# Kernel optimization log

Measured on AMD Instinct MI355X. Metric: run time of the kernel, lower is better.

Reference implementation:

```python
import jax, jax.numpy as jnp
import numpy as np

N, E = 50000, 500000
D_NODE, D_EDGE, N_REL, N_CLS = 128, 128, 64, 16


def setup_inputs() -> dict:
    key = jax.random.key(0)
    ks = jax.random.split(key, 16)
    cat = 2 * D_NODE + D_EDGE  # 384
    s = 0.05
    return {
        "node_features": jax.random.normal(ks[0], (N, D_NODE), jnp.float32),
        "edge_features": jax.random.normal(ks[1], (E, D_EDGE), jnp.float32),
        "edge_index": jax.random.randint(ks[2], (2, E), 0, N, jnp.int32),
        "labels_for_rel_emb": jax.random.randint(ks[3], (E,), 0, N_REL, jnp.int32),
        "rel_emb": jax.random.normal(ks[4], (N_REL, D_EDGE), jnp.float32) * s,
        "msg_W": jax.random.normal(ks[5], (D_NODE, cat), jnp.float32) * s,
        "msg_b": jnp.zeros((D_NODE,), jnp.float32),
        "gru_w_ih": jax.random.normal(ks[6], (3 * D_NODE, D_NODE), jnp.float32) * s,
        "gru_w_hh": jax.random.normal(ks[7], (3 * D_NODE, D_NODE), jnp.float32) * s,
        "gru_b_ih": jnp.zeros((3 * D_NODE,), jnp.float32),
        "gru_b_hh": jnp.zeros((3 * D_NODE,), jnp.float32),
        "cls_W1": jax.random.normal(ks[8], (D_EDGE, cat), jnp.float32) * s,
        "cls_b1": jnp.zeros((D_EDGE,), jnp.float32),
        "cls_W2": jax.random.normal(ks[9], (N_CLS, D_EDGE), jnp.float32) * s,
        "cls_b2": jnp.zeros((N_CLS,), jnp.float32),
    }


def reference(node_features, edge_features, edge_index, labels_for_rel_emb,
              rel_emb, msg_W, msg_b, gru_w_ih, gru_w_hh, gru_b_ih, gru_b_hh,
              cls_W1, cls_b1, cls_W2, cls_b2):
    src, tgt = edge_index[0], edge_index[1]
    nf = node_features
    rel_feat = rel_emb[labels_for_rel_emb]                      # [E, d_edge]
    h = jnp.concatenate([nf[src], nf[tgt], rel_feat], axis=-1)  # [E, 384]
    msg = jax.nn.gelu(h @ msg_W.T + msg_b, approximate=False)   # [E, d_node]
    agg = jax.ops.segment_sum(msg, tgt, num_segments=nf.shape[0])  # [N, d_node]
    # torch.nn.GRUCell(agg, nf)
    gi = agg @ gru_w_ih.T + gru_b_ih
    gh = nf @ gru_w_hh.T + gru_b_hh
    i_r, i_z, i_n = jnp.split(gi, 3, axis=-1)
    h_r, h_z, h_n = jnp.split(gh, 3, axis=-1)
    r = jax.nn.sigmoid(i_r + h_r)
    z = jax.nn.sigmoid(i_z + h_z)
    n = jnp.tanh(i_n + r * h_n)
    nf_u = (1.0 - z) * n + z * nf
    c = jnp.concatenate([nf_u[src], nf_u[tgt], edge_features], axis=-1)  # [E, 384]
    hc = jax.nn.gelu(c @ cls_W1.T + cls_b1, approximate=False)           # [E, d_edge]
    return hc @ cls_W2.T + cls_b2                                        # [E, num_classes]
```

## Files before the change

kernel.cpp:

```cpp
#include <hip/hip_runtime.h>
#include <math.h>

#define N_NODES 50000
#define N_EDGES 500000
#define D 128
#define CAT 384

typedef __bf16 v8bf __attribute__((ext_vector_type(8)));
typedef __bf16 v2bf __attribute__((ext_vector_type(2)));
typedef float v4f __attribute__((ext_vector_type(4)));

__device__ __forceinline__ float erf_fast(float x) {
    float ax = fabsf(x);
    float t = __builtin_amdgcn_rcpf(fmaf(0.3275911f, ax, 1.0f));
    float p = fmaf(1.061405429f, t, -1.453152027f);
    p = fmaf(p, t, 1.421413741f);
    p = fmaf(p, t, -0.284496736f);
    p = fmaf(p, t, 0.254829592f);
    p = p * t;
    float e = __expf(-ax * ax);
    float r = 1.0f - p * e;
    return copysignf(r, x);
}

__device__ __forceinline__ float gelu_fast(float x) {
    return 0.5f * x * (1.0f + erf_fast(x * 0.70710678118654752440f));
}

__device__ __forceinline__ float sigmoid_fast(float x) {
    float e = __expf(-x);
    return __builtin_amdgcn_rcpf(1.0f + e);
}

__device__ __forceinline__ float tanh_fast(float x) {
    float e = __expf(2.0f * x);
    return 1.0f - 2.0f * __builtin_amdgcn_rcpf(e + 1.0f);
}

__device__ __forceinline__ v8bf cvt8(const float* __restrict__ p) {
    float4 f0 = *(const float4*)p;
    float4 f1 = *(const float4*)(p + 4);
    v8bf r;
    r[0] = (__bf16)f0.x; r[1] = (__bf16)f0.y; r[2] = (__bf16)f0.z; r[3] = (__bf16)f0.w;
    r[4] = (__bf16)f1.x; r[5] = (__bf16)f1.y; r[6] = (__bf16)f1.z; r[7] = (__bf16)f1.w;
    return r;
}

__global__ __launch_bounds__(256) void k_zero(int* __restrict__ counts) {
    int i = blockIdx.x * 256 + threadIdx.x;
    if (i < N_NODES) counts[i] = 0;
}

__global__ __launch_bounds__(256) void k_pre(const float* __restrict__ msgW,
                                             const float* __restrict__ W1,
                                             const float* __restrict__ W2,
                                             const float* __restrict__ wih,
                                             const float* __restrict__ whh,
                                             __bf16* __restrict__ WB,
                                             const float* __restrict__ rel_emb,
                                             const float* __restrict__ msg_b,
                                             __bf16* __restrict__ RPB,
                                             const int* __restrict__ ei,
                                             int* __restrict__ counts) {
    int bid = blockIdx.x;
    int t = threadIdx.x;
    if (bid < 712) {
        int i = bid * 256 + t;
        float v;
        if (i < 32768) {
            int j = i >> 7, k = i & 127;
            v = (j < 128) ? msgW[j * CAT + k] : msgW[(j - 128) * CAT + 128 + k];
        } else if (i < 65536) {
            int ii = i - 32768; int j = ii >> 7, k = ii & 127;
            v = (j < 128) ? W1[j * CAT + k] : W1[(j - 128) * CAT + 128 + k];
        } else if (i < 81920) {
            int ii = i - 65536; int j = ii >> 7, k = ii & 127;
            v = W1[j * CAT + 256 + k];
        } else if (i < 83968) {
            v = W2[i - 81920];
        } else if (i < 133120) {
            v = wih[i - 83968];
        } else {
            v = whh[i - 133120];
        }
        WB[i] = (__bf16)v;
    } else if (bid < 744) {
        int r = (bid - 712) * 2 + (t >> 7);
        int j = t & 127;
        const float* er = rel_emb + r * D;
        const float* wr = msgW + j * CAT + 2 * D;
        float acc = msg_b[j];
        #pragma unroll 8
        for (int k = 0; k < D; ++k) acc += er[k] * wr[k];
        RPB[r * D + j] = (__bf16)acc;
    } else {
        int e = (bid - 744) * 256 + t;
        if (e < N_EDGES) atomicAdd(&counts[ei[N_EDGES + e]], 1);
    }
}

__global__ __launch_bounds__(256) void k_proj2_f32(const float* __restrict__ in,
                                                   const __bf16* __restrict__ wb,
                                                   __bf16* __restrict__ out) {
    int t = threadIdx.x;
    int lane = t & 63, wid = t >> 6;
    int g = lane >> 4, c = lane & 15;
    int nbase = blockIdx.x * 64 + wid * 16;

    int nrow = min(nbase + c, N_NODES - 1);
    const float* ir = in + (size_t)nrow * D + g * 8;
    v8bf afrag[4];
    #pragma unroll
    for (int kc = 0; kc < 4; ++kc) afrag[kc] = cvt8(ir + kc * 32);

    #pragma unroll
    for (int half = 0; half < 2; ++half) {
        v4f acc[8];
        #pragma unroll 2
        for (int jt = 0; jt < 8; ++jt) {
            const __bf16* wr = wb + (size_t)(half * 128 + 8 * c + jt) * 128 + g * 8;
            v4f a4 = (v4f){0.f, 0.f, 0.f, 0.f};
            #pragma unroll
            for (int kc = 0; kc < 4; ++kc)
                a4 = __builtin_amdgcn_mfma_f32_16x16x32_bf16(afrag[kc], *(const v8bf*)(wr + kc * 32), a4, 0, 0, 0);
            acc[jt] = a4;
        }
        #pragma unroll
        for (int r = 0; r < 4; ++r) {
            int node = nbase + g * 4 + r;
            v8bf o;
            #pragma unroll
            for (int jt = 0; jt < 8; ++jt) o[jt] = (__bf16)acc[jt][r];
            if (node < N_NODES)
                *(v8bf*)(out + (size_t)node * 256 + half * 128 + 8 * c) = o;
        }
    }
}

__global__ __launch_bounds__(256) void k_proj2_b16(const __bf16* __restrict__ in,
                                                   const __bf16* __restrict__ wb,
                                                   __bf16* __restrict__ out) {
    int t = threadIdx.x;
    int lane = t & 63, wid = t >> 6;
    int g = lane >> 4, c = lane & 15;
    int nbase = blockIdx.x * 64 + wid * 16;

    int nrow = min(nbase + c, N_NODES - 1);
    const __bf16* ir = in + (size_t)nrow * D + g * 8;
    v8bf afrag[4];
    #pragma unroll
    for (int kc = 0; kc < 4; ++kc) afrag[kc] = *(const v8bf*)(ir + kc * 32);

    #pragma unroll
    for (int half = 0; half < 2; ++half) {
        v4f acc[8];
        #pragma unroll 2
        for (int jt = 0; jt < 8; ++jt) {
            const __bf16* wr = wb + (size_t)(half * 128 + 8 * c + jt) * 128 + g * 8;
            v4f a4 = (v4f){0.f, 0.f, 0.f, 0.f};
            #pragma unroll
            for (int kc = 0; kc < 4; ++kc)
                a4 = __builtin_amdgcn_mfma_f32_16x16x32_bf16(afrag[kc], *(const v8bf*)(wr + kc * 32), a4, 0, 0, 0);
            acc[jt] = a4;
        }
        #pragma unroll
        for (int r = 0; r < 4; ++r) {
            int node = nbase + g * 4 + r;
            v8bf o;
            #pragma unroll
            for (int jt = 0; jt < 8; ++jt) o[jt] = (__bf16)acc[jt][r];
            if (node < N_NODES)
                *(v8bf*)(out + (size_t)node * 256 + half * 128 + 8 * c) = o;
        }
    }
}

__global__ __launch_bounds__(1024) void k_scan(const int* __restrict__ counts,
                                               int* __restrict__ offsets,
                                               int* __restrict__ cursor) {
    __shared__ int part[1024];
    int t = threadIdx.x;
    const int CH = 49;
    int lo = t * CH, hi = min(lo + CH, N_NODES);
    int s = 0;
    for (int i = lo; i < hi; ++i) s += counts[i];
    part[t] = s;
    __syncthreads();
    for (int d = 1; d < 1024; d <<= 1) {
        int v = (t >= d) ? part[t - d] : 0;
        __syncthreads();
        part[t] += v;
        __syncthreads();
    }
    int run = (t == 0) ? 0 : part[t - 1];
    for (int i = lo; i < hi; ++i) {
        offsets[i] = run;
        cursor[i] = run;
        run += counts[i];
    }
    if (t == 1023) offsets[N_NODES] = run;
}

__global__ __launch_bounds__(256) void k_scatter(const int* __restrict__ ei,
                                                 int* __restrict__ cursor,
                                                 int* __restrict__ elist) {
    int e = blockIdx.x * 256 + threadIdx.x;
    if (e < N_EDGES) {
        int slot = atomicAdd(&cursor[ei[N_EDGES + e]], 1);
        elist[slot] = e;
    }
}

__global__ __launch_bounds__(256) void k_agg(const __bf16* __restrict__ PSTB,
                                             const __bf16* __restrict__ RPB,
                                             const int* __restrict__ ei,
                                             const int* __restrict__ lab,
                                             const int* __restrict__ offsets,
                                             const int* __restrict__ elist,
                                             __bf16* __restrict__ agg) {
    int t = threadIdx.x;
    int wid = t >> 6, lane = t & 63;
    int n = blockIdx.x * 4 + wid;
    if (n >= N_NODES) return;
    int beg = offsets[n], end = offsets[n + 1];

    v2bf ptv = *(const v2bf*)(PSTB + (size_t)n * 256 + 128 + lane * 2);
    float pt0 = (float)ptv[0], pt1 = (float)ptv[1];

    float a0 = 0.f, a1 = 0.f;
    if (beg < end) {
        int mx = end - 1;
        int eA = elist[beg];
        int eB = elist[min(beg + 1, mx)];
        int e2 = elist[min(beg + 2, mx)];
        int e3 = elist[min(beg + 3, mx)];
        int sA = ei[eA], lA = lab[eA];
        int sB = ei[eB], lB = lab[eB];
        int s2 = ei[e2], l2 = lab[e2];
        int s3 = ei[e3], l3 = lab[e3];
        v2bf psA = *(const v2bf*)(PSTB + (size_t)sA * 256 + lane * 2);
        v2bf rpA = *(const v2bf*)(RPB + (size_t)lA * D + lane * 2);
        v2bf psB = *(const v2bf*)(PSTB + (size_t)sB * 256 + lane * 2);
        v2bf rpB = *(const v2bf*)(RPB + (size_t)lB * D + lane * 2);

        for (int idx = beg; idx < end; idx += 2) {
            v2bf cpsA = psA, crpA = rpA, cpsB = psB, crpB = rpB;
            bool hasB = (idx + 1 < end);
            psA = *(const v2bf*)(PSTB + (size_t)s2 * 256 + lane * 2);
            rpA = *(const v2bf*)(RPB + (size_t)l2 * D + lane * 2);
            psB = *(const v2bf*)(PSTB + (size_t)s3 * 256 + lane * 2);
            rpB = *(const v2bf*)(RPB + (size_t)l3 * D + lane * 2);
            int e4 = elist[min(idx + 4, mx)];
            int e5 = elist[min(idx + 5, mx)];
            s2 = ei[e4]; l2 = lab[e4];
            s3 = ei[e5]; l3 = lab[e5];
            a0 += gelu_fast((float)cpsA[0] + pt0 + (float)crpA[0]);
            a1 += gelu_fast((float)cpsA[1] + pt1 + (float)crpA[1]);
            if (hasB) {
                a0 += gelu_fast((float)cpsB[0] + pt0 + (float)crpB[0]);
                a1 += gelu_fast((float)cpsB[1] + pt1 + (float)crpB[1]);
            }
        }
    }
    v2bf o; o[0] = (__bf16)a0; o[1] = (__bf16)a1;
    *(v2bf*)(agg + (size_t)n * D + lane * 2) = o;
}

__global__ __launch_bounds__(256) void k_gru_mfma(const __bf16* __restrict__ agg,
                                                  const float* __restrict__ nf,
                                                  const __bf16* __restrict__ WIH,
                                                  const __bf16* __restrict__ WHH,
                                                  const float* __restrict__ b_ih,
                                                  const float* __restrict__ b_hh,
                                                  __bf16* __restrict__ nfu) {
    int t = threadIdx.x;
    int lane = t & 63, wid = t >> 6;
    int g = lane >> 4, c = lane & 15;
    int nbase = blockIdx.x * 64 + wid * 16;

    int nrow = min(nbase + c, N_NODES - 1);
    const __bf16* ar = agg + (size_t)nrow * D + g * 8;
    const float* hr = nf + (size_t)nrow * D + g * 8;
    v8bf afrag[4], hfrag[4];
    #pragma unroll
    for (int kc = 0; kc < 4; ++kc) {
        afrag[kc] = *(const v8bf*)(ar + kc * 32);
        hfrag[kc] = cvt8(hr + kc * 32);
    }

    float h8[4][8];
    #pragma unroll
    for (int r = 0; r < 4; ++r) {
        int node = min(nbase + g * 4 + r, N_NODES - 1);
        float4 f0 = *(const float4*)(nf + (size_t)node * D + 8 * c);
        float4 f1 = *(const float4*)(nf + (size_t)node * D + 8 * c + 4);
        h8[r][0]=f0.x; h8[r][1]=f0.y; h8[r][2]=f0.z; h8[r][3]=f0.w;
        h8[r][4]=f1.x; h8[r][5]=f1.y; h8[r][6]=f1.z; h8[r][7]=f1.w;
    }

    v8bf o[4];
    for (int jt = 0; jt < 8; ++jt) {
        int j = 8 * c + jt;
        const __bf16* wir = WIH + (size_t)j * 128 + g * 8;
        const __bf16* whr = WHH + (size_t)j * 128 + g * 8;
        v4f a_ir = (v4f){0.f,0.f,0.f,0.f}, a_iz = a_ir, a_in = a_ir;
        v4f a_hr = a_ir, a_hz = a_ir, a_hn = a_ir;
        #pragma unroll
        for (int kc = 0; kc < 4; ++kc) {
            a_ir = __builtin_amdgcn_mfma_f32_16x16x32_bf16(afrag[kc], *(const v8bf*)(wir + kc * 32), a_ir, 0, 0, 0);
            a_iz = __builtin_amdgcn_mfma_f32_16x16x32_bf16(afrag[kc], *(const v8bf*)(wir + 128 * 128 + kc * 32), a_iz, 0, 0, 0);
            a_in = __builtin_amdgcn_mfma_f32_16x16x32_bf16(afrag[kc], *(const v8bf*)(wir + 256 * 128 + kc * 32), a_in, 0, 0, 0);
            a_hr = __builtin_amdgcn_mfma_f32_16x16x32_bf16(hfrag[kc], *(const v8bf*)(whr + kc * 32), a_hr, 0, 0, 0);
            a_hz = __builtin_amdgcn_mfma_f32_16x16x32_bf16(hfrag[kc], *(const v8bf*)(whr + 128 * 128 + kc * 32), a_hz, 0, 0, 0);
            a_hn = __builtin_amdgcn_mfma_f32_16x16x32_bf16(hfrag[kc], *(const v8bf*)(whr + 256 * 128 + kc * 32), a_hn, 0, 0, 0);
        }
        float bir = b_ih[j], biz = b_ih[128 + j], bin = b_ih[256 + j];
        float bhr = b_hh[j], bhz = b_hh[128 + j], bhn = b_hh[256 + j];
        #pragma unroll
        for (int r = 0; r < 4; ++r) {
            float irv = a_ir[r] + bir, hrv = a_hr[r] + bhr;
            float izv = a_iz[r] + biz, hzv = a_hz[r] + bhz;
            float inv = a_in[r] + bin, hnv = a_hn[r] + bhn;
            float rg = sigmoid_fast(irv + hrv);
            float zg = sigmoid_fast(izv + hzv);
            float ng = tanh_fast(inv + rg * hnv);
            o[r][jt] = (__bf16)((1.f - zg) * ng + zg * h8[r][jt]);
        }
    }
    #pragma unroll
    for (int r = 0; r < 4; ++r) {
        int node = nbase + g * 4 + r;
        if (node < N_NODES) *(v8bf*)(nfu + (size_t)node * D + 8 * c) = o[r];
    }
}

__global__ __launch_bounds__(256) void k_cls_mfma(const float* __restrict__ ef,
                                                  const __bf16* __restrict__ QSTB,
                                                  const __bf16* __restrict__ V3,
                                                  const float* __restrict__ b1,
                                                  const __bf16* __restrict__ W2B,
                                                  const float* __restrict__ b2,
                                                  const int* __restrict__ ei,
                                                  float* __restrict__ out) {
    __shared__ __align__(16) __bf16 v3_s[128][128];
    __shared__ __align__(16) __bf16 hc_s[64][128];
    int t = threadIdx.x;
    int lane = t & 63, w = t >> 6;
    int g = lane >> 4, c = lane & 15;
    const int ntile = (N_EDGES + 63) / 64;

    int tile = blockIdx.x;
    int sr[4], tr[4];
    float4 efraw[8];
    if (tile < ntile) {
        int e_base = tile * 64 + w * 16;
        int er = min(e_base + c, N_EDGES - 1);
        const float* efr = ef + (size_t)er * D + g * 8;
        #pragma unroll
        for (int kc = 0; kc < 4; ++kc) {
            efraw[2 * kc]     = *(const float4*)(efr + kc * 32);
            efraw[2 * kc + 1] = *(const float4*)(efr + kc * 32 + 4);
        }
        #pragma unroll
        for (int r = 0; r < 4; ++r) {
            int e = min(e_base + g * 4 + r, N_EDGES - 1);
            sr[r] = ei[e];
            tr[r] = ei[N_EDGES + e];
        }
    }

    v8bf w2frag[4];
    #pragma unroll
    for (int kc = 0; kc < 4; ++kc)
        w2frag[kc] = *(const v8bf*)(W2B + c * 128 + (g + 4 * kc) * 8);
    float4 b1a = *(const float4*)(b1 + 8 * c);
    float4 b1b = *(const float4*)(b1 + 8 * c + 4);
    float b1r[8] = {b1a.x, b1a.y, b1a.z, b1a.w, b1b.x, b1b.y, b1b.z, b1b.w};
    float b2c = b2[c];

    #pragma unroll
    for (int i = 0; i < 8; ++i) {
        int idx = t * 8 + i;
        int row = idx >> 4, ch = idx & 15;
        v8bf v = *(const v8bf*)(V3 + row * 128 + ch * 8);
        *(v8bf*)&v3_s[row][8 * (ch ^ ((row >> 3) & 7))] = v;
    }
    __syncthreads();

    while (tile < ntile) {
        int next = tile + gridDim.x;
        int e_base = tile * 64 + w * 16;

        v8bf qsv[4], qtv[4];
        #pragma unroll
        for (int r = 0; r < 4; ++r) {
            qsv[r] = *(const v8bf*)(QSTB + (size_t)sr[r] * 256 + 8 * c);
            qtv[r] = *(const v8bf*)(QSTB + (size_t)tr[r] * 256 + 128 + 8 * c);
        }

        v8bf afrag[4];
        #pragma unroll
        for (int kc = 0; kc < 4; ++kc) {
            v8bf a;
            float4 f0 = efraw[2 * kc], f1 = efraw[2 * kc + 1];
            a[0] = (__bf16)f0.x; a[1] = (__bf16)f0.y; a[2] = (__bf16)f0.z; a[3] = (__bf16)f0.w;
            a[4] = (__bf16)f1.x; a[5] = (__bf16)f1.y; a[6] = (__bf16)f1.z; a[7] = (__bf16)f1.w;
            afrag[kc] = a;
        }

        int sr_n[4], tr_n[4];
        if (next < ntile) {
            int nb = next * 64 + w * 16;
            int er = min(nb + c, N_EDGES - 1);
            const float* efr = ef + (size_t)er * D + g * 8;
            #pragma unroll
            for (int kc = 0; kc < 4; ++kc) {
                efraw[2 * kc]     = *(const float4*)(efr + kc * 32);
                efraw[2 * kc + 1] = *(const float4*)(efr + kc * 32 + 4);
            }
            #pragma unroll
            for (int r = 0; r < 4; ++r) {
                int e = min(nb + g * 4 + r, N_EDGES - 1);
                sr_n[r] = ei[e];
                tr_n[r] = ei[N_EDGES + e];
            }
        }

        v4f acc[8];
        #pragma unroll
        for (int jt = 0; jt < 8; ++jt) {
            int row = 8 * c + jt;
            v4f a4 = (v4f){0.f, 0.f, 0.f, 0.f};
            #pragma unroll
            for (int kc = 0; kc < 4; ++kc) {
                v8bf bb = *(const v8bf*)&v3_s[row][8 * ((g + 4 * kc) ^ (c & 7))];
                a4 = __builtin_amdgcn_mfma_f32_16x16x32_bf16(afrag[kc], bb, a4, 0, 0, 0);
            }
            acc[jt] = a4;
        }

        #pragma unroll
        for (int r = 0; r < 4; ++r) {
            int el = w * 16 + g * 4 + r;
            v8bf o;
            #pragma unroll
            for (int jt = 0; jt < 8; ++jt) {
                float v = acc[jt][r] + (float)qsv[r][jt] + (float)qtv[r][jt] + b1r[jt];
                o[jt] = (__bf16)gelu_fast(v);
            }
            *(v8bf*)&hc_s[el][8 * (c ^ (el & 7))] = o;
        }

        v4f acc2 = (v4f){0.f, 0.f, 0.f, 0.f};
        int arow = w * 16 + c;
        #pragma unroll
        for (int kc = 0; kc < 4; ++kc) {
            int ch = g + 4 * kc;
            v8bf aa = *(const v8bf*)&hc_s[arow][8 * (ch ^ (c & 7))];
            acc2 = __builtin_amdgcn_mfma_f32_16x16x32_bf16(aa, w2frag[kc], acc2, 0, 0, 0);
        }
        #pragma unroll
        for (int r = 0; r < 4; ++r) {
            int e = e_base + g * 4 + r;
            if (e < N_EDGES) out[(size_t)e * 16 + c] = acc2[r] + b2c;
        }

        #pragma unroll
        for (int r = 0; r < 4; ++r) { sr[r] = sr_n[r]; tr[r] = tr_n[r]; }
        tile = next;
    }
}

extern "C" void kernel_launch(void* const* d_in, const int* in_sizes, int n_in,
                              void* d_out, int out_size, void* d_ws, size_t ws_size,
                              hipStream_t stream) {
    const float* nf   = (const float*)d_in[0];
    const float* ef   = (const float*)d_in[1];
    const int*   ei   = (const int*)d_in[2];
    const int*   lab  = (const int*)d_in[3];
    const float* rel  = (const float*)d_in[4];
    const float* msgW = (const float*)d_in[5];
    const float* msgb = (const float*)d_in[6];
    const float* wih  = (const float*)d_in[7];
    const float* whh  = (const float*)d_in[8];
    const float* bih  = (const float*)d_in[9];
    const float* bhh  = (const float*)d_in[10];
    const float* W1   = (const float*)d_in[11];
    const float* b1   = (const float*)d_in[12];
    const float* W2   = (const float*)d_in[13];
    const float* b2   = (const float*)d_in[14];
    float* out = (float*)d_out;

    char* ws = (char*)d_ws;
    __bf16* WB      = (__bf16*)(ws);
    __bf16* RPB     = (__bf16*)(ws + 524288);
    int*    offsets = (int*)(ws + 1048576);
    int*    counts  = (int*)(ws + 1310720);
    int*    cursor  = (int*)(ws + 1572864);
    int*    elist   = (int*)(ws + 1835008);
    __bf16* PSTB    = (__bf16*)(ws + 4194304);
    __bf16* AGG     = (__bf16*)(ws + 33554432);
    __bf16* NFUB    = (__bf16*)(ws + 50331648);
    __bf16* QSTB    = PSTB;

    __bf16* WP1 = WB;
    __bf16* WQ1 = WB + 32768;
    __bf16* V3  = WB + 65536;
    __bf16* W2B = WB + 81920;
    __bf16* WIH = WB + 83968;
    __bf16* WHH = WB + 133120;

    int nblk = (N_NODES + 63) / 64;
    int eblk = (N_EDGES + 255) / 256;

    k_zero<<<(N_NODES + 255) / 256, 256, 0, stream>>>(counts);
    k_pre<<<744 + eblk, 256, 0, stream>>>(msgW, W1, W2, wih, whh, WB,
                                          rel, msgb, RPB, ei, counts);
    k_proj2_f32<<<nblk, 256, 0, stream>>>(nf, WP1, PSTB);
    k_scan<<<1, 1024, 0, stream>>>(counts, offsets, cursor);
    k_scatter<<<eblk, 256, 0, stream>>>(ei, cursor, elist);
    k_agg<<<(N_NODES + 3) / 4, 256, 0, stream>>>(PSTB, RPB, ei, lab, offsets, elist, AGG);
    k_gru_mfma<<<nblk, 256, 0, stream>>>(AGG, nf, WIH, WHH, bih, bhh, NFUB);
    k_proj2_b16<<<nblk, 256, 0, stream>>>(NFUB, WQ1, QSTB);
    k_cls_mfma<<<768, 256, 0, stream>>>(ef, QSTB, V3, b1, W2B, b2, ei, out);
}
```

Before: 511.1 us.

## Fuse GRU update with node projection and deepen gather prefetch in classifier

The GRU kernel now keeps each 64-node tile of updated node features in swizzled shared memory and immediately runs the Q projection MFMA on it. This removes the separate projection kernel and the global round trip of the intermediate nfu buffer. The classifier kernel is also reworked to prefetch edge indices two tiles ahead and the gathered QSTB rows one tile ahead, hiding gather latency behind the MFMA work. The cost is higher register pressure and extra shared memory in the fused GRU kernel.

```diff
diff --git a/kernel.cpp b/kernel.cpp
--- a/kernel.cpp
+++ b/kernel.cpp
@@ -137,44 +137,6 @@
     }
 }
 
-__global__ __launch_bounds__(256) void k_proj2_b16(const __bf16* __restrict__ in,
-                                                   const __bf16* __restrict__ wb,
-                                                   __bf16* __restrict__ out) {
-    int t = threadIdx.x;
-    int lane = t & 63, wid = t >> 6;
-    int g = lane >> 4, c = lane & 15;
-    int nbase = blockIdx.x * 64 + wid * 16;
-
-    int nrow = min(nbase + c, N_NODES - 1);
-    const __bf16* ir = in + (size_t)nrow * D + g * 8;
-    v8bf afrag[4];
-    #pragma unroll
-    for (int kc = 0; kc < 4; ++kc) afrag[kc] = *(const v8bf*)(ir + kc * 32);
-
-    #pragma unroll
-    for (int half = 0; half < 2; ++half) {
-        v4f acc[8];
-        #pragma unroll 2
-        for (int jt = 0; jt < 8; ++jt) {
-            const __bf16* wr = wb + (size_t)(half * 128 + 8 * c + jt) * 128 + g * 8;
-            v4f a4 = (v4f){0.f, 0.f, 0.f, 0.f};
-            #pragma unroll
-            for (int kc = 0; kc < 4; ++kc)
-                a4 = __builtin_amdgcn_mfma_f32_16x16x32_bf16(afrag[kc], *(const v8bf*)(wr + kc * 32), a4, 0, 0, 0);
-            acc[jt] = a4;
-        }
-        #pragma unroll
-        for (int r = 0; r < 4; ++r) {
-            int node = nbase + g * 4 + r;
-            v8bf o;
-            #pragma unroll
-            for (int jt = 0; jt < 8; ++jt) o[jt] = (__bf16)acc[jt][r];
-            if (node < N_NODES)
-                *(v8bf*)(out + (size_t)node * 256 + half * 128 + 8 * c) = o;
-        }
-    }
-}
-
 __global__ __launch_bounds__(1024) void k_scan(const int* __restrict__ counts,
                                                int* __restrict__ offsets,
                                                int* __restrict__ cursor) {
@@ -266,13 +228,15 @@
     *(v2bf*)(agg + (size_t)n * D + lane * 2) = o;
 }
 
-__global__ __launch_bounds__(256) void k_gru_mfma(const __bf16* __restrict__ agg,
-                                                  const float* __restrict__ nf,
-                                                  const __bf16* __restrict__ WIH,
-                                                  const __bf16* __restrict__ WHH,
-                                                  const float* __restrict__ b_ih,
-                                                  const float* __restrict__ b_hh,
-                                                  __bf16* __restrict__ nfu) {
+__global__ __launch_bounds__(256) void k_gru_fused(const __bf16* __restrict__ agg,
+                                                   const float* __restrict__ nf,
+                                                   const __bf16* __restrict__ WIH,
+                                                   const __bf16* __restrict__ WHH,
+                                                   const float* __restrict__ b_ih,
+                                                   const float* __restrict__ b_hh,
+                                                   const __bf16* __restrict__ WQ1,
+                                                   __bf16* __restrict__ QSTB) {
+    __shared__ __align__(16) __bf16 nfu_s[64][128];
     int t = threadIdx.x;
     int lane = t & 63, wid = t >> 6;
     int g = lane >> 4, c = lane & 15;
@@ -329,8 +293,37 @@
     }
     #pragma unroll
     for (int r = 0; r < 4; ++r) {
-        int node = nbase + g * 4 + r;
-        if (node < N_NODES) *(v8bf*)(nfu + (size_t)node * D + 8 * c) = o[r];
+        int lr = wid * 16 + g * 4 + r;
+        *(v8bf*)&nfu_s[lr][8 * (c ^ (lr & 7))] = o[r];
+    }
+
+    int lr2 = wid * 16 + c;
+    v8bf pfrag[4];
+    #pragma unroll
+    for (int kc = 0; kc < 4; ++kc)
+        pfrag[kc] = *(const v8bf*)&nfu_s[lr2][8 * ((g + 4 * kc) ^ (c & 7))];
+
+    #pragma unroll
+    for (int half = 0; half < 2; ++half) {
+        v4f acc[8];
+        #pragma unroll 2
+        for (int jt = 0; jt < 8; ++jt) {
+            const __bf16* wr = WQ1 + (size_t)(half * 128 + 8 * c + jt) * 128 + g * 8;
+            v4f a4 = (v4f){0.f, 0.f, 0.f, 0.f};
+            #pragma unroll
+            for (int kc = 0; kc < 4; ++kc)
+                a4 = __builtin_amdgcn_mfma_f32_16x16x32_bf16(pfrag[kc], *(const v8bf*)(wr + kc * 32), a4, 0, 0, 0);
+            acc[jt] = a4;
+        }
+        #pragma unroll
+        for (int r = 0; r < 4; ++r) {
+            int node = nbase + g * 4 + r;
+            v8bf oo;
+            #pragma unroll
+            for (int jt = 0; jt < 8; ++jt) oo[jt] = (__bf16)acc[jt][r];
+            if (node < N_NODES)
+                *(v8bf*)(QSTB + (size_t)node * 256 + half * 128 + 8 * c) = oo;
+        }
     }
 }
 
@@ -348,26 +341,9 @@
     int lane = t & 63, w = t >> 6;
     int g = lane >> 4, c = lane & 15;
     const int ntile = (N_EDGES + 63) / 64;
+    const int stride = gridDim.x;
 
     int tile = blockIdx.x;
-    int sr[4], tr[4];
-    float4 efraw[8];
-    if (tile < ntile) {
-        int e_base = tile * 64 + w * 16;
-        int er = min(e_base + c, N_EDGES - 1);
-        const float* efr = ef + (size_t)er * D + g * 8;
-        #pragma unroll
-        for (int kc = 0; kc < 4; ++kc) {
-            efraw[2 * kc]     = *(const float4*)(efr + kc * 32);
-            efraw[2 * kc + 1] = *(const float4*)(efr + kc * 32 + 4);
-        }
-        #pragma unroll
-        for (int r = 0; r < 4; ++r) {
-            int e = min(e_base + g * 4 + r, N_EDGES - 1);
-            sr[r] = ei[e];
-            tr[r] = ei[N_EDGES + e];
-        }
-    }
 
     v8bf w2frag[4];
     #pragma unroll
@@ -378,6 +354,25 @@
     float b1r[8] = {b1a.x, b1a.y, b1a.z, b1a.w, b1b.x, b1b.y, b1b.z, b1b.w};
     float b2c = b2[c];
 
+    float4 efraw[8];
+    int sr[4], tr[4];
+    {
+        int e_base = tile * 64 + w * 16;
+        int er = min(e_base + c, N_EDGES - 1);
+        const float* efr = ef + (size_t)er * D + g * 8;
+        #pragma unroll
+        for (int kc = 0; kc < 4; ++kc) {
+            efraw[2 * kc]     = *(const float4*)(efr + kc * 32);
+            efraw[2 * kc + 1] = *(const float4*)(efr + kc * 32 + 4);
+        }
+        #pragma unroll
+        for (int r = 0; r < 4; ++r) {
+            int e = min(e_base + g * 4 + r, N_EDGES - 1);
+            sr[r] = ei[e];
+            tr[r] = ei[N_EDGES + e];
+        }
+    }
+
     #pragma unroll
     for (int i = 0; i < 8; ++i) {
         int idx = t * 8 + i;
@@ -387,16 +382,26 @@
     }
     __syncthreads();
 
+    v8bf qs[4], qt[4];
+    #pragma unroll
+    for (int r = 0; r < 4; ++r) {
+        qs[r] = *(const v8bf*)(QSTB + (size_t)sr[r] * 256 + 8 * c);
+        qt[r] = *(const v8bf*)(QSTB + (size_t)tr[r] * 256 + 128 + 8 * c);
+    }
+    int srn[4], trn[4];
+    if (tile + stride < ntile) {
+        int nb = (tile + stride) * 64 + w * 16;
+        #pragma unroll
+        for (int r = 0; r < 4; ++r) {
+            int e = min(nb + g * 4 + r, N_EDGES - 1);
+            srn[r] = ei[e];
+            trn[r] = ei[N_EDGES + e];
+        }
+    }
+
     while (tile < ntile) {
-        int next = tile + gridDim.x;
+        int nxt = tile + stride;
         int e_base = tile * 64 + w * 16;
-
-        v8bf qsv[4], qtv[4];
-        #pragma unroll
-        for (int r = 0; r < 4; ++r) {
-            qsv[r] = *(const v8bf*)(QSTB + (size_t)sr[r] * 256 + 8 * c);
-            qtv[r] = *(const v8bf*)(QSTB + (size_t)tr[r] * 256 + 128 + 8 * c);
-        }
 
         v8bf afrag[4];
         #pragma unroll
@@ -408,9 +413,8 @@
             afrag[kc] = a;
         }
 
-        int sr_n[4], tr_n[4];
-        if (next < ntile) {
-            int nb = next * 64 + w * 16;
+        if (nxt < ntile) {
+            int nb = nxt * 64 + w * 16;
             int er = min(nb + c, N_EDGES - 1);
             const float* efr = ef + (size_t)er * D + g * 8;
             #pragma unroll
@@ -418,11 +422,24 @@
                 efraw[2 * kc]     = *(const float4*)(efr + kc * 32);
                 efraw[2 * kc + 1] = *(const float4*)(efr + kc * 32 + 4);
             }
+        }
+
+        v8bf qsn[4], qtn[4];
+        if (nxt < ntile) {
+            #pragma unroll
+            for (int r = 0; r < 4; ++r) {
+                qsn[r] = *(const v8bf*)(QSTB + (size_t)srn[r] * 256 + 8 * c);
+                qtn[r] = *(const v8bf*)(QSTB + (size_t)trn[r] * 256 + 128 + 8 * c);
+            }
+        }
+
+        if (nxt + stride < ntile) {
+            int nb = (nxt + stride) * 64 + w * 16;
             #pragma unroll
             for (int r = 0; r < 4; ++r) {
                 int e = min(nb + g * 4 + r, N_EDGES - 1);
-                sr_n[r] = ei[e];
-                tr_n[r] = ei[N_EDGES + e];
+                srn[r] = ei[e];
+                trn[r] = ei[N_EDGES + e];
             }
         }
 
@@ -445,7 +462,7 @@
             v8bf o;
             #pragma unroll
             for (int jt = 0; jt < 8; ++jt) {
-                float v = acc[jt][r] + (float)qsv[r][jt] + (float)qtv[r][jt] + b1r[jt];
+                float v = acc[jt][r] + (float)qs[r][jt] + (float)qt[r][jt] + b1r[jt];
                 o[jt] = (__bf16)gelu_fast(v);
             }
             *(v8bf*)&hc_s[el][8 * (c ^ (el & 7))] = o;
@@ -466,8 +483,8 @@
         }
 
         #pragma unroll
-        for (int r = 0; r < 4; ++r) { sr[r] = sr_n[r]; tr[r] = tr_n[r]; }
-        tile = next;
+        for (int r = 0; r < 4; ++r) { qs[r] = qsn[r]; qt[r] = qtn[r]; }
+        tile = nxt;
     }
 }
 
@@ -500,7 +517,6 @@
     int*    elist   = (int*)(ws + 1835008);
     __bf16* PSTB    = (__bf16*)(ws + 4194304);
     __bf16* AGG     = (__bf16*)(ws + 33554432);
-    __bf16* NFUB    = (__bf16*)(ws + 50331648);
     __bf16* QSTB    = PSTB;
 
     __bf16* WP1 = WB;
@@ -520,7 +536,6 @@
     k_scan<<<1, 1024, 0, stream>>>(counts, offsets, cursor);
     k_scatter<<<eblk, 256, 0, stream>>>(ei, cursor, elist);
     k_agg<<<(N_NODES + 3) / 4, 256, 0, stream>>>(PSTB, RPB, ei, lab, offsets, elist, AGG);
-    k_gru_mfma<<<nblk, 256, 0, stream>>>(AGG, nf, WIH, WHH, bih, bhh, NFUB);
-    k_proj2_b16<<<nblk, 256, 0, stream>>>(NFUB, WQ1, QSTB);
+    k_gru_fused<<<nblk, 256, 0, stream>>>(AGG, nf, WIH, WHH, bih, bhh, WQ1, QSTB);
     k_cls_mfma<<<768, 256, 0, stream>>>(ef, QSTB, V3, b1, W2B, b2, ei, out);
 }
```

Result: no change. 511.3 us, median of 2 (+0.0%).
